# Performance work log

Hardware: AMD Instinct MI355X
Metric: run time of the kernel (lower is better)

The kernel has to match this reference:

```python
import jax, jax.numpy as jnp
import numpy as np
from jax import lax

SIGMAS = [0.5, 1.0, 2.0]
CHANNELS = 64

def _gaussian_kernel(sigma, channels):
    k = int(6 * sigma + 1) | 1
    x = np.arange(k, dtype=np.float32) - k // 2
    k1 = np.exp(-x ** 2 / (2 * sigma ** 2))
    k2 = np.outer(k1, k1)
    k2 = k2 / k2.sum()
    # depthwise weight layout OIHW with feature_group_count=channels: (C, 1, k, k)
    w = np.broadcast_to(k2[None, None], (channels, 1, k, k)).copy()
    return jnp.asarray(w)

_KERNELS = [_gaussian_kernel(s, CHANNELS) for s in SIGMAS]

def setup_inputs() -> dict:
    key = jax.random.key(0)
    k1, k2, k3 = jax.random.split(key, 3)
    x = jax.random.normal(k1, (8, CHANNELS, 256, 256), dtype=jnp.float32)
    fusion_w = jax.random.normal(k2, (CHANNELS, CHANNELS * len(SIGMAS)), dtype=jnp.float32) * 0.05
    fusion_b = jax.random.normal(k3, (CHANNELS,), dtype=jnp.float32) * 0.05
    return {"x": x, "fusion_w": fusion_w, "fusion_b": fusion_b}

def _depthwise(x, w):
    return lax.conv_general_dilated(
        x, w, window_strides=(1, 1), padding="SAME",
        dimension_numbers=("NCHW", "OIHW", "NCHW"),
        feature_group_count=x.shape[1])

def reference(x, fusion_w, fusion_b):
    # multi-scale depthwise Gaussian blurs, concat on channel dim
    multi_scale = jnp.concatenate([_depthwise(x, w) for w in _KERNELS], axis=1)  # [B, 3C, H, W]
    # 1x1 fusion conv + bias
    fused = jnp.einsum("bchw,oc->bohw", multi_scale, fusion_w) + fusion_b[None, :, None, None]
    return x + fused
```

## Files before the change

kernel.cpp:

```cpp
#include <hip/hip_runtime.h>
#include <hip/hip_bf16.h>
#include <math.h>

#define B_  8
#define C_  64
#define H_  256
#define W_  256
#define HW_ (H_*W_)
#define J_  192

typedef __attribute__((ext_vector_type(8))) short short8;
typedef __attribute__((ext_vector_type(4))) float f32x4;

__device__ __forceinline__ ushort f2bf(float f) {
    union { float f; uint u; } v; v.f = f;
    uint u = v.u;
    return (ushort)((u + 0x7fffu + ((u >> 16) & 1u)) >> 16);
}
__device__ __forceinline__ float bf2f(ushort s) {
    union { uint u; float f; } v; v.u = ((uint)s) << 16;
    return v.f;
}
__device__ __forceinline__ uint pk(float a, float b) {
    return (uint)f2bf(a) | ((uint)f2bf(b) << 16);
}
__device__ __forceinline__ float bflo(uint u) {
    union { uint u; float f; } v; v.u = u << 16; return v.f;
}
__device__ __forceinline__ float bfhi(uint u) {
    union { uint u; float f; } v; v.u = u & 0xffff0000u; return v.f;
}

__global__ __launch_bounds__(256) void k1_mix(
    const float* __restrict__ x, const float* __restrict__ fw,
    ushort* __restrict__ v)
{
    __shared__ ushort lxs[256 * 64];

    const int b      = blockIdx.x >> 8;
    const int pxbase = (blockIdx.x & 255) << 8;
    const int t      = threadIdx.x;
    const int lane   = t & 63;
    const int wv_    = t >> 6;

    {
        const int cg = lane;
        const float* xb = x + (size_t)b * C_ * HW_ + pxbase + 4 * cg;
#pragma unroll
        for (int i = 0; i < 4; ++i) {
            const int cb = wv_ * 4 + i * 16;
            const int c4 = wv_ + i * 4;
            float4 r0 = *(const float4*)(xb + (size_t)(cb + 0) * HW_);
            float4 r1 = *(const float4*)(xb + (size_t)(cb + 1) * HW_);
            float4 r2 = *(const float4*)(xb + (size_t)(cb + 2) * HW_);
            float4 r3 = *(const float4*)(xb + (size_t)(cb + 3) * HW_);
            const int sbase = c4 ^ (cg & 15);
            ushort* dst = &lxs[(4 * cg) * 64];
            *(uint2*)(dst + 0*64 + ((sbase ^ 0) * 4)) = make_uint2(pk(r0.x, r1.x), pk(r2.x, r3.x));
            *(uint2*)(dst + 1*64 + ((sbase ^ 4) * 4)) = make_uint2(pk(r0.y, r1.y), pk(r2.y, r3.y));
            *(uint2*)(dst + 2*64 + ((sbase ^ 8) * 4)) = make_uint2(pk(r0.z, r1.z), pk(r2.z, r3.z));
            *(uint2*)(dst + 3*64 + ((sbase ^ 12) * 4)) = make_uint2(pk(r0.w, r1.w), pk(r2.w, r3.w));
        }
    }

    const int n = lane & 15;
    const int q = lane >> 4;
    union Frag { short8 v; uint u[4]; };
    Frag wf[3][2];
#pragma unroll
    for (int i = 0; i < 3; ++i) {
        const int j  = (wv_ * 3 + i) * 16 + n;
        const float* wr = fw + (size_t)(j & 63) * J_ + (j >> 6) * 64;
#pragma unroll
        for (int kh = 0; kh < 2; ++kh) {
            float4 w0 = *(const float4*)(wr + kh * 32 + q * 8);
            float4 w1 = *(const float4*)(wr + kh * 32 + q * 8 + 4);
            wf[i][kh].u[0] = pk(w0.x, w0.y);
            wf[i][kh].u[1] = pk(w0.z, w0.w);
            wf[i][kh].u[2] = pk(w1.x, w1.y);
            wf[i][kh].u[3] = pk(w1.z, w1.w);
        }
    }

    __syncthreads();

    for (int mt = 0; mt < 16; ++mt) {
        const int px = mt * 16 + (lane & 15);
        const ushort* row = &lxs[px * 64];
        const int s = ((px >> 2) & 15) ^ ((px & 3) << 2);
        Frag a0, a1;
        {
            uint2 lo  = *(const uint2*)&row[((2*q    ) ^ s) * 4];
            uint2 hi  = *(const uint2*)&row[((2*q + 1) ^ s) * 4];
            a0.u[0] = lo.x;  a0.u[1] = lo.y;  a0.u[2] = hi.x;  a0.u[3] = hi.y;
            uint2 lo1 = *(const uint2*)&row[((8 + 2*q    ) ^ s) * 4];
            uint2 hi1 = *(const uint2*)&row[((8 + 2*q + 1) ^ s) * 4];
            a1.u[0] = lo1.x; a1.u[1] = lo1.y; a1.u[2] = hi1.x; a1.u[3] = hi1.y;
        }
#pragma unroll
        for (int i = 0; i < 3; ++i) {
            f32x4 acc = {0.f, 0.f, 0.f, 0.f};
            acc = __builtin_amdgcn_mfma_f32_16x16x32_bf16(a0.v, wf[i][0].v, acc, 0, 0, 0);
            acc = __builtin_amdgcn_mfma_f32_16x16x32_bf16(a1.v, wf[i][1].v, acc, 0, 0, 0);
            const int j   = (wv_ * 3 + i) * 16 + n;
            const int pxg = pxbase + mt * 16 + q * 4;
            *(uint2*)&v[(size_t)(b * J_ + j) * HW_ + pxg] =
                make_uint2(pk(acc[0], acc[1]), pk(acc[2], acc[3]));
        }
    }
}

#define TH2_ 16
#define TROWS_ (TH2_+4 + TH2_+6 + TH2_+12)

struct Taps {
    float g0[5];
    float g1[7];
    float g2[13];
};

template<int R, int G>
__device__ __forceinline__ void hjob(
    const ushort* __restrict__ vplane, const float* __restrict__ g,
    ushort* __restrict__ dstrow, int gh, int cg)
{
    const int NG  = 2 * G + 1;
    const int OFF = 4 * G - R;
    const int K   = 2 * R + 1;
    float o0 = 0.f, o1 = 0.f, o2 = 0.f, o3 = 0.f;
    if (gh >= 0 && gh < H_) {
        const ushort* vr = vplane + (size_t)gh * W_;
        float win[NG * 4];
#pragma unroll
        for (int gi = 0; gi < NG; ++gi) {
            const int gg = cg - G + gi;
            uint2 d = (gg >= 0 && gg < 64) ? *(const uint2*)(vr + gg * 4)
                                           : make_uint2(0u, 0u);
            win[gi*4+0] = bflo(d.x); win[gi*4+1] = bfhi(d.x);
            win[gi*4+2] = bflo(d.y); win[gi*4+3] = bfhi(d.y);
        }
#pragma unroll
        for (int dd = 0; dd < K; ++dd) {
            const float gd = g[dd];
            o0 += gd * win[OFF + dd + 0];
            o1 += gd * win[OFF + dd + 1];
            o2 += gd * win[OFF + dd + 2];
            o3 += gd * win[OFF + dd + 3];
        }
    }
    *(uint2*)&dstrow[4 * cg] = make_uint2(pk(o0, o1), pk(o2, o3));
}

template<int R>
__device__ __forceinline__ void vjob(
    const ushort* __restrict__ tmp0, const float* __restrict__ g,
    int cg, float4* acc)
{
#pragma unroll
    for (int k = 0; k < 4 + 2 * R; ++k) {
        uint2 raw = *(const uint2*)&tmp0[k * W_ + 4 * cg];
        const float f0 = bflo(raw.x), f1 = bfhi(raw.x);
        const float f2 = bflo(raw.y), f3 = bfhi(raw.y);
        const int ilo = (k - 2 * R) > 0 ? (k - 2 * R) : 0;
        const int ihi = k < 3 ? k : 3;
#pragma unroll
        for (int i = ilo; i <= ihi; ++i) {
            const float gd = g[k - i];
            acc[i].x += gd * f0;
            acc[i].y += gd * f1;
            acc[i].z += gd * f2;
            acc[i].w += gd * f3;
        }
    }
}

__global__ __launch_bounds__(256, 4) void k2_blur(
    const ushort* __restrict__ v, const float* __restrict__ x,
    const float* __restrict__ bias, float* __restrict__ out,
    Taps taps)
{
    __shared__ ushort tmp[TROWS_ * W_];

    const int t    = blockIdx.x;
    const int tile = t & 15;
    const int o    = (t >> 4) & 63;
    const int b    = t >> 10;
    const int h0   = tile * TH2_;
    const int cg   = threadIdx.x & 63;
    const int rw   = threadIdx.x >> 6;
    const int c0   = cg * 4;

    const ushort* vp = v + (size_t)(b * J_ + o) * HW_;

    for (int r = rw; r < TH2_ + 4; r += 4)
        hjob<2, 1>(vp,                        taps.g0, &tmp[r * W_],            h0 - 2 + r, cg);
    for (int r = rw; r < TH2_ + 6; r += 4)
        hjob<3, 1>(vp + (size_t)C_ * HW_,     taps.g1, &tmp[(20 + r) * W_],     h0 - 3 + r, cg);
    for (int r = rw; r < TH2_ + 12; r += 4)
        hjob<6, 2>(vp + (size_t)(2*C_) * HW_, taps.g2, &tmp[(42 + r) * W_],     h0 - 6 + r, cg);

    __syncthreads();

    float4 acc[4];
#pragma unroll
    for (int i = 0; i < 4; ++i) acc[i] = make_float4(0.f, 0.f, 0.f, 0.f);

    vjob<2>(&tmp[(0  + rw * 4) * W_], taps.g0, cg, acc);
    vjob<3>(&tmp[(20 + rw * 4) * W_], taps.g1, cg, acc);
    vjob<6>(&tmp[(42 + rw * 4) * W_], taps.g2, cg, acc);

    const int row0 = h0 + rw * 4;
    const float* xp = x   + ((size_t)b * C_ + o) * HW_ + (size_t)row0 * W_;
    float*       op = out + ((size_t)b * C_ + o) * HW_ + (size_t)row0 * W_;
    const float bo = bias[o];
#pragma unroll
    for (int i = 0; i < 4; ++i) {
        float4 xv = *(const float4*)&xp[(size_t)i * W_ + c0];
        float4 r;
        r.x = xv.x + bo + acc[i].x;
        r.y = xv.y + bo + acc[i].y;
        r.z = xv.z + bo + acc[i].z;
        r.w = xv.w + bo + acc[i].w;
        *(float4*)&op[(size_t)i * W_ + c0] = r;
    }
}

static void make_taps(Taps& t)
{
    auto fill = [](float* g, int k, double sigma) {
        int r = k / 2;
        double s = 0.0;
        for (int i = 0; i < k; ++i) {
            double w = exp(-(double)((i - r) * (i - r)) / (2.0 * sigma * sigma));
            g[i] = (float)w;
            s += w;
        }
        for (int i = 0; i < k; ++i) g[i] = (float)((double)g[i] / s);
    };
    fill(t.g0, 5, 0.5);
    fill(t.g1, 7, 1.0);
    fill(t.g2, 13, 2.0);
}

extern "C" void kernel_launch(void* const* d_in, const int* in_sizes, int n_in,
                              void* d_out, int out_size, void* d_ws, size_t ws_size,
                              hipStream_t stream)
{
    const float* x  = (const float*)d_in[0];
    const float* fw = (const float*)d_in[1];
    const float* fb = (const float*)d_in[2];
    float* out = (float*)d_out;
    ushort* v = (ushort*)d_ws;

    Taps taps;
    make_taps(taps);

    k1_mix<<<dim3(B_ * (HW_ / 256)), dim3(256), 0, stream>>>(x, fw, v);
    k2_blur<<<dim3(B_ * C_ * (H_ / TH2_)), dim3(256), 0, stream>>>(v, x, fb, out, taps);
}
```

Measured before the change: 432.4 us.

## Compute vertical blur pass with MFMA banded matrices on transposed LDS tiles

The horizontal blur pass now writes its results transposed into per-column-group LDS tiles, with each thread handling four rows and using clamped offsets plus masks instead of branches. The vertical blur is then done as MFMA products against banded Gaussian matrices, built in registers and split into hi/lo bf16 parts to keep precision. This replaces the scalar FMA vertical convolution and its many LDS reads, at the cost of more LDS, lower occupancy (launch bounds 4 to 3), and extra MFMAs for the split weights.

```diff
diff --git a/kernel.cpp b/kernel.cpp
--- a/kernel.cpp
+++ b/kernel.cpp
@@ -8,6 +8,7 @@
 #define W_  256
 #define HW_ (H_*W_)
 #define J_  192
+#define TH2_ 16
 
 typedef __attribute__((ext_vector_type(8))) short short8;
 typedef __attribute__((ext_vector_type(4))) float f32x4;
@@ -110,124 +111,192 @@
     }
 }
 
-#define TH2_ 16
-#define TROWS_ (TH2_+4 + TH2_+6 + TH2_+12)
+#define COL01  24
+#define TIL01  392
+#define COL2   40
+#define TIL2   648
+#define S0B    0
+#define S1B    (16*TIL01)
+#define S2B    (2*16*TIL01)
+#define LDSTOT (S2B + 16*TIL2)
 
 struct Taps {
     float g0[5];
     float g1[7];
     float g2[13];
+    float ke[3];
+    float cn[3];
 };
 
-template<int R, int G>
-__device__ __forceinline__ void hjob(
+union BF8 { short8 v; uint u[4]; };
+
+template<int R>
+__device__ __forceinline__ void make_gband(float ke, float cn, int n, int q,
+                                           BF8& hi, BF8& lo)
+{
+    float val[8];
+#pragma unroll
+    for (int e = 0; e < 8; ++e) {
+        const int kk = 8 * q + e;
+        const int d  = kk - n;
+        float vv = 0.f;
+        if (d >= 0 && d <= 2*R) {
+            const int dist = d - R;
+            vv = exp2f(-(float)(dist*dist) * ke) * cn;
+        }
+        val[e] = vv;
+    }
+#pragma unroll
+    for (int i = 0; i < 4; ++i) {
+        const ushort h0 = f2bf(val[2*i]);
+        const ushort h1 = f2bf(val[2*i+1]);
+        hi.u[i] = (uint)h0 | ((uint)h1 << 16);
+        lo.u[i] = pk(val[2*i] - bf2f(h0), val[2*i+1] - bf2f(h1));
+    }
+}
+
+template<int R, int G, int NROWS, int CUS>
+__device__ __forceinline__ void hjob4(
     const ushort* __restrict__ vplane, const float* __restrict__ g,
-    ushort* __restrict__ dstrow, int gh, int cg)
-{
-    const int NG  = 2 * G + 1;
-    const int OFF = 4 * G - R;
-    const int K   = 2 * R + 1;
-    float o0 = 0.f, o1 = 0.f, o2 = 0.f, o3 = 0.f;
-    if (gh >= 0 && gh < H_) {
-        const ushort* vr = vplane + (size_t)gh * W_;
-        float win[NG * 4];
+    ushort* __restrict__ lds, int tbase, int h0, int qd, int cg,
+    const int* coff, const uint* cmsk)
+{
+    constexpr int NG = 2*G + 1, K = 2*R + 1, OFF = 4*G - R;
+    float o[4][4];
+#pragma unroll
+    for (int rr = 0; rr < 4; ++rr) {
+        const int r  = 4*qd + rr;
+        const int gh = h0 - R + r;
+        const int ghc = gh < 0 ? 0 : (gh > H_-1 ? H_-1 : gh);
+        const float rv = (gh >= 0 && gh < H_ && r < NROWS) ? 1.f : 0.f;
+        const char* vr = (const char*)(vplane + (size_t)ghc * W_);
+        uint2 raw[NG];
+#pragma unroll
+        for (int gi = 0; gi < NG; ++gi)
+            raw[gi] = *(const uint2*)(vr + coff[gi]);
+        float win[NG*4];
 #pragma unroll
         for (int gi = 0; gi < NG; ++gi) {
-            const int gg = cg - G + gi;
-            uint2 d = (gg >= 0 && gg < 64) ? *(const uint2*)(vr + gg * 4)
-                                           : make_uint2(0u, 0u);
-            win[gi*4+0] = bflo(d.x); win[gi*4+1] = bfhi(d.x);
-            win[gi*4+2] = bflo(d.y); win[gi*4+3] = bfhi(d.y);
-        }
-#pragma unroll
-        for (int dd = 0; dd < K; ++dd) {
-            const float gd = g[dd];
-            o0 += gd * win[OFF + dd + 0];
-            o1 += gd * win[OFF + dd + 1];
-            o2 += gd * win[OFF + dd + 2];
-            o3 += gd * win[OFF + dd + 3];
-        }
-    }
-    *(uint2*)&dstrow[4 * cg] = make_uint2(pk(o0, o1), pk(o2, o3));
-}
-
-template<int R>
-__device__ __forceinline__ void vjob(
-    const ushort* __restrict__ tmp0, const float* __restrict__ g,
-    int cg, float4* acc)
-{
-#pragma unroll
-    for (int k = 0; k < 4 + 2 * R; ++k) {
-        uint2 raw = *(const uint2*)&tmp0[k * W_ + 4 * cg];
-        const float f0 = bflo(raw.x), f1 = bfhi(raw.x);
-        const float f2 = bflo(raw.y), f3 = bfhi(raw.y);
-        const int ilo = (k - 2 * R) > 0 ? (k - 2 * R) : 0;
-        const int ihi = k < 3 ? k : 3;
-#pragma unroll
-        for (int i = ilo; i <= ihi; ++i) {
-            const float gd = g[k - i];
-            acc[i].x += gd * f0;
-            acc[i].y += gd * f1;
-            acc[i].z += gd * f2;
-            acc[i].w += gd * f3;
-        }
-    }
-}
-
-__global__ __launch_bounds__(256, 4) void k2_blur(
+            const uint dx = raw[gi].x & cmsk[gi];
+            const uint dy = raw[gi].y & cmsk[gi];
+            win[gi*4+0] = bflo(dx); win[gi*4+1] = bfhi(dx);
+            win[gi*4+2] = bflo(dy); win[gi*4+3] = bfhi(dy);
+        }
+#pragma unroll
+        for (int i2 = 0; i2 < 4; ++i2) {
+            float s = 0.f;
+#pragma unroll
+            for (int dd = 0; dd < K; ++dd) s += g[dd] * win[OFF + dd + i2];
+            o[rr][i2] = s * rv;
+        }
+    }
+    ushort* base = lds + tbase + 4*qd;
+#pragma unroll
+    for (int i2 = 0; i2 < 4; ++i2) {
+        *(uint2*)&base[(4*(cg&3) + i2) * CUS] =
+            make_uint2(pk(o[0][i2], o[1][i2]), pk(o[2][i2], o[3][i2]));
+    }
+}
+
+__global__ __launch_bounds__(256, 3) void k2_blur(
     const ushort* __restrict__ v, const float* __restrict__ x,
     const float* __restrict__ bias, float* __restrict__ out,
     Taps taps)
 {
-    __shared__ ushort tmp[TROWS_ * W_];
+    __shared__ ushort tmp2[LDSTOT];
 
     const int t    = blockIdx.x;
     const int tile = t & 15;
     const int o    = (t >> 4) & 63;
     const int b    = t >> 10;
     const int h0   = tile * TH2_;
-    const int cg   = threadIdx.x & 63;
-    const int rw   = threadIdx.x >> 6;
-    const int c0   = cg * 4;
+    const int tid  = threadIdx.x;
+    const int cg   = tid & 63;
+    const int rw   = tid >> 6;
+
+    int coff1[3]; uint cm1[3];
+    int coff2[5]; uint cm2[5];
+#pragma unroll
+    for (int gi = 0; gi < 3; ++gi) {
+        const int gg = cg - 1 + gi;
+        const int gc = gg < 0 ? 0 : (gg > 63 ? 63 : gg);
+        coff1[gi] = gc * 8;
+        cm1[gi]   = (gg == gc) ? 0xffffffffu : 0u;
+    }
+#pragma unroll
+    for (int gi = 0; gi < 5; ++gi) {
+        const int gg = cg - 2 + gi;
+        const int gc = gg < 0 ? 0 : (gg > 63 ? 63 : gg);
+        coff2[gi] = gc * 8;
+        cm2[gi]   = (gg == gc) ? 0xffffffffu : 0u;
+    }
 
     const ushort* vp = v + (size_t)(b * J_ + o) * HW_;
-
-    for (int r = rw; r < TH2_ + 4; r += 4)
-        hjob<2, 1>(vp,                        taps.g0, &tmp[r * W_],            h0 - 2 + r, cg);
-    for (int r = rw; r < TH2_ + 6; r += 4)
-        hjob<3, 1>(vp + (size_t)C_ * HW_,     taps.g1, &tmp[(20 + r) * W_],     h0 - 3 + r, cg);
-    for (int r = rw; r < TH2_ + 12; r += 4)
-        hjob<6, 2>(vp + (size_t)(2*C_) * HW_, taps.g2, &tmp[(42 + r) * W_],     h0 - 6 + r, cg);
+    const int tb01 = (cg >> 2) * TIL01;
+    const int tb2  = (cg >> 2) * TIL2;
+
+    hjob4<2,1,20,COL01>(vp, taps.g0, tmp2, S0B + tb01, h0, rw,     cg, coff1, cm1);
+    if (tid < 128)
+        hjob4<2,1,20,COL01>(vp, taps.g0, tmp2, S0B + tb01, h0, rw + 4, cg, coff1, cm1);
+    hjob4<3,1,22,COL01>(vp + (size_t)C_ * HW_, taps.g1, tmp2, S1B + tb01, h0, rw,     cg, coff1, cm1);
+    if (tid >= 128)
+        hjob4<3,1,22,COL01>(vp + (size_t)C_ * HW_, taps.g1, tmp2, S1B + tb01, h0, rw + 2, cg, coff1, cm1);
+    hjob4<6,2,28,COL2>(vp + (size_t)(2*C_) * HW_, taps.g2, tmp2, S2B + tb2, h0, rw,     cg, coff2, cm2);
+    hjob4<6,2,28,COL2>(vp + (size_t)(2*C_) * HW_, taps.g2, tmp2, S2B + tb2, h0, rw + 4, cg, coff2, cm2);
+
+    const int lane = tid & 63;
+    const int n2 = lane & 15;
+    const int q2 = lane >> 4;
+    BF8 g0h, g0l, g1h, g1l, g2h, g2l;
+    make_gband<2>(taps.ke[0], taps.cn[0], n2, q2, g0h, g0l);
+    make_gband<3>(taps.ke[1], taps.cn[1], n2, q2, g1h, g1l);
+    make_gband<6>(taps.ke[2], taps.cn[2], n2, q2, g2h, g2l);
 
     __syncthreads();
 
-    float4 acc[4];
-#pragma unroll
-    for (int i = 0; i < 4; ++i) acc[i] = make_float4(0.f, 0.f, 0.f, 0.f);
-
-    vjob<2>(&tmp[(0  + rw * 4) * W_], taps.g0, cg, acc);
-    vjob<3>(&tmp[(20 + rw * 4) * W_], taps.g1, cg, acc);
-    vjob<6>(&tmp[(42 + rw * 4) * W_], taps.g2, cg, acc);
-
-    const int row0 = h0 + rw * 4;
-    const float* xp = x   + ((size_t)b * C_ + o) * HW_ + (size_t)row0 * W_;
-    float*       op = out + ((size_t)b * C_ + o) * HW_ + (size_t)row0 * W_;
+    const uint zm = (q2 == 3) ? 0u : 0xffffffffu;
+    const int qs = (q2 == 3) ? 0 : q2;
     const float bo = bias[o];
+    const size_t obase = ((size_t)b * C_ + o) * HW_;
+
 #pragma unroll
     for (int i = 0; i < 4; ++i) {
-        float4 xv = *(const float4*)&xp[(size_t)i * W_ + c0];
-        float4 r;
-        r.x = xv.x + bo + acc[i].x;
-        r.y = xv.y + bo + acc[i].y;
-        r.z = xv.z + bo + acc[i].z;
-        r.w = xv.w + bo + acc[i].w;
-        *(float4*)&op[(size_t)i * W_ + c0] = r;
+        const int mt = rw * 4 + i;
+        uint4 d0 = *(const uint4*)&tmp2[S0B + mt*TIL01 + n2*COL01 + 8*qs];
+        uint4 d1 = *(const uint4*)&tmp2[S1B + mt*TIL01 + n2*COL01 + 8*qs];
+        uint4 d2 = *(const uint4*)&tmp2[S2B + mt*TIL2  + n2*COL2  + 8*q2];
+        d0.x &= zm; d0.y &= zm; d0.z &= zm; d0.w &= zm;
+        d1.x &= zm; d1.y &= zm; d1.z &= zm; d1.w &= zm;
+
+        BF8 a0, a1, a2;
+        a0.u[0] = d0.x; a0.u[1] = d0.y; a0.u[2] = d0.z; a0.u[3] = d0.w;
+        a1.u[0] = d1.x; a1.u[1] = d1.y; a1.u[2] = d1.z; a1.u[3] = d1.w;
+        a2.u[0] = d2.x; a2.u[1] = d2.y; a2.u[2] = d2.z; a2.u[3] = d2.w;
+
+        f32x4 acc = {0.f, 0.f, 0.f, 0.f};
+        acc = __builtin_amdgcn_mfma_f32_16x16x32_bf16(a0.v, g0h.v, acc, 0, 0, 0);
+        acc = __builtin_amdgcn_mfma_f32_16x16x32_bf16(a0.v, g0l.v, acc, 0, 0, 0);
+        acc = __builtin_amdgcn_mfma_f32_16x16x32_bf16(a1.v, g1h.v, acc, 0, 0, 0);
+        acc = __builtin_amdgcn_mfma_f32_16x16x32_bf16(a1.v, g1l.v, acc, 0, 0, 0);
+        acc = __builtin_amdgcn_mfma_f32_16x16x32_bf16(a2.v, g2h.v, acc, 0, 0, 0);
+        acc = __builtin_amdgcn_mfma_f32_16x16x32_bf16(a2.v, g2l.v, acc, 0, 0, 0);
+
+        const int orow = h0 + n2;
+        const int ocol = mt * 16 + 4 * q2;
+        const float* xp = x + obase + (size_t)orow * W_ + ocol;
+        float4 xv = *(const float4*)xp;
+        float4 rr;
+        rr.x = xv.x + bo + acc[0];
+        rr.y = xv.y + bo + acc[1];
+        rr.z = xv.z + bo + acc[2];
+        rr.w = xv.w + bo + acc[3];
+        *(float4*)(out + obase + (size_t)orow * W_ + ocol) = rr;
     }
 }
 
 static void make_taps(Taps& t)
 {
-    auto fill = [](float* g, int k, double sigma) {
+    auto fill = [](float* g, int k, double sigma, float* ke, float* cn) {
         int r = k / 2;
         double s = 0.0;
         for (int i = 0; i < k; ++i) {
@@ -236,10 +305,12 @@
             s += w;
         }
         for (int i = 0; i < k; ++i) g[i] = (float)((double)g[i] / s);
+        *ke = (float)(1.4426950408889634 / (2.0 * sigma * sigma));
+        *cn = (float)(1.0 / s);
     };
-    fill(t.g0, 5, 0.5);
-    fill(t.g1, 7, 1.0);
-    fill(t.g2, 13, 2.0);
+    fill(t.g0, 5,  0.5, &t.ke[0], &t.cn[0]);
+    fill(t.g1, 7,  1.0, &t.ke[1], &t.cn[1]);
+    fill(t.g2, 13, 2.0, &t.ke[2], &t.cn[2]);
 }
 
 extern "C" void kernel_launch(void* const* d_in, const int* in_sizes, int n_in,
```

New measurement: 424.6 us. No clear change (-1.8%).
